# Kernel optimization log

Measured on AMD Instinct MI355X. Metric: run time of the kernel, lower is better.

## Reference

```python
import jax, jax.numpy as jnp
import numpy as np

N_NODES = 50000
N_EDGES = 20000
EDGE_SIZE = 32
IN_CH = 256
OUT_CH = 256


def setup_inputs() -> dict:
    key = jax.random.key(0)
    k1, k2, k3 = jax.random.split(key, 3)
    x = jax.random.normal(k1, (N_NODES, IN_CH), dtype=jnp.float32)
    hyperedges = jax.random.randint(k2, (N_EDGES, EDGE_SIZE), 0, N_NODES)
    weight = jax.random.normal(k3, (IN_CH, OUT_CH), dtype=jnp.float32)
    return {"x": x, "hyperedges": hyperedges, "weight": weight}


def reference(x, hyperedges, weight):
    # Gather node features per hyperedge and reduce ('sum' aggregation):
    # [E, K, C] -> [E, C]
    edge_sum = x[hyperedges].sum(axis=1)
    # Scatter-add each hyperedge's summed feature back to every member node.
    agg = jnp.zeros_like(x).at[hyperedges].add(edge_sum[:, None, :])
    # Dense projection + ReLU.
    return jax.nn.relu(agg @ weight)
```

## Files before the change

kernel.cpp:

```cpp
#include <hip/hip_runtime.h>
#include <hip/hip_bf16.h>

#define N_NODES 50000
#define N_EDGES 20000
#define EDGE_K  32
#define CH      256
#define N_INC   (N_EDGES * EDGE_K)
#define ELL_CAP 64

typedef __attribute__((ext_vector_type(4))) float f32x4;
typedef __attribute__((ext_vector_type(8))) short bf16x8;

static __device__ __forceinline__ unsigned short f2bf(float f) {
    __hip_bfloat16 h = __float2bfloat16(f);
    return *reinterpret_cast<unsigned short*>(&h);
}

static __device__ __forceinline__ float bf2f(unsigned short u) {
    unsigned int b = ((unsigned int)u) << 16;
    float f;
    __builtin_memcpy(&f, &b, 4);
    return f;
}

#define CONV_BLOCKS ((N_NODES * CH / 4 + 255) / 256)
#define ZERO_BLOCKS ((N_NODES + 255) / 256)
__global__ void prep_kernel(const float* __restrict__ x, unsigned short* __restrict__ xb,
                            const float* __restrict__ w, unsigned short* __restrict__ wt,
                            int* __restrict__ deg) {
    int b = blockIdx.x;
    if (b < CONV_BLOCKS) {
        int i = b * 256 + threadIdx.x;
        if (i < N_NODES * CH / 4) {
            f32x4 v = reinterpret_cast<const f32x4*>(x)[i];
            ushort4 s;
            s.x = f2bf(v.x);
            s.y = f2bf(v.y);
            s.z = f2bf(v.z);
            s.w = f2bf(v.w);
            reinterpret_cast<ushort4*>(xb)[i] = s;
        }
    } else if (b < CONV_BLOCKS + CH) {
        int n = b - CONV_BLOCKS;
        int k = threadIdx.x;
        wt[n * CH + k] = f2bf(w[k * CH + n]);
    } else {
        int i = (b - CONV_BLOCKS - CH) * 256 + threadIdx.x;
        if (i < N_NODES) deg[i] = 0;
    }
}

#define GATHER_BLOCKS ((N_EDGES + 3) / 4)
#define FILL_BLOCKS   ((N_INC + 255) / 256)
__global__ void gather_fill_kernel(const unsigned short* __restrict__ xb,
                                   const int* __restrict__ he,
                                   unsigned short* __restrict__ es,
                                   int* __restrict__ deg,
                                   unsigned short* __restrict__ ell) {
    int b = blockIdx.x;
    if (b < GATHER_BLOCKS) {
        int wave = b * 4 + (threadIdx.x >> 6);
        int lane = threadIdx.x & 63;
        if (wave >= N_EDGES) return;
        int myidx = he[wave * EDGE_K + (lane & 31)];
        const ushort4* xb4 = reinterpret_cast<const ushort4*>(xb);
        f32x4 acc = {0.f, 0.f, 0.f, 0.f};
#pragma unroll
        for (int k = 0; k < EDGE_K; ++k) {
            int e = __shfl(myidx, k, 64);
            ushort4 v = xb4[(size_t)e * (CH / 4) + lane];
            acc.x += bf2f(v.x);
            acc.y += bf2f(v.y);
            acc.z += bf2f(v.z);
            acc.w += bf2f(v.w);
        }
        ushort4 s;
        s.x = f2bf(acc.x);
        s.y = f2bf(acc.y);
        s.z = f2bf(acc.z);
        s.w = f2bf(acc.w);
        reinterpret_cast<ushort4*>(es + (size_t)wave * CH)[lane] = s;
    } else {
        int i = (b - GATHER_BLOCKS) * 256 + threadIdx.x;
        if (i >= N_INC) return;
        int node = he[i];
        int slot = atomicAdd(&deg[node], 1);
        if (slot < ELL_CAP) ell[(size_t)node * ELL_CAP + slot] = (unsigned short)(i >> 5);
    }
}

__global__ __launch_bounds__(256) void gemm_kernel(const unsigned short* __restrict__ es,
                                                   const unsigned short* __restrict__ wt,
                                                   unsigned short* __restrict__ yb) {
    int wid  = threadIdx.x >> 6;
    int lane = threadIdx.x & 63;
    int m0   = blockIdx.x * 64 + wid * 16;
    if (m0 >= N_EDGES) return;
    int lr = lane & 15;
    int lg = lane >> 4;

    f32x4 acc[16] = {};

    const unsigned short* arow = es + (size_t)(m0 + lr) * CH + lg * 8;
#pragma unroll
    for (int kk = 0; kk < CH; kk += 32) {
        bf16x8 a = *reinterpret_cast<const bf16x8*>(arow + kk);
#pragma unroll
        for (int nt = 0; nt < 16; ++nt) {
            bf16x8 b = *reinterpret_cast<const bf16x8*>(
                wt + (size_t)(nt * 16 + lr) * CH + kk + lg * 8);
            acc[nt] = __builtin_amdgcn_mfma_f32_16x16x32_bf16(a, b, acc[nt], 0, 0, 0);
        }
    }

#pragma unroll
    for (int nt = 0; nt < 16; ++nt) {
#pragma unroll
        for (int r = 0; r < 4; ++r) {
            yb[(size_t)(m0 + lg * 4 + r) * CH + nt * 16 + lr] = f2bf(acc[nt][r]);
        }
    }
}

__global__ void apply_kernel(const unsigned short* __restrict__ yb, const int* __restrict__ deg,
                             const unsigned short* __restrict__ ell, float* __restrict__ out) {
    int node = (int)((blockIdx.x * blockDim.x + threadIdx.x) >> 6);
    int lane = threadIdx.x & 63;
    if (node >= N_NODES) return;
    int d = deg[node];
    if (d > ELL_CAP) d = ELL_CAP;
    int myidx = (int)ell[(size_t)node * ELL_CAP + lane];
    const ushort4* yb4 = reinterpret_cast<const ushort4*>(yb);
    f32x4 acc = {0.f, 0.f, 0.f, 0.f};
    int j = 0;
    for (; j + 4 <= d; j += 4) {
        int e0 = __shfl(myidx, j + 0, 64);
        int e1 = __shfl(myidx, j + 1, 64);
        int e2 = __shfl(myidx, j + 2, 64);
        int e3 = __shfl(myidx, j + 3, 64);
        ushort4 v0 = yb4[(size_t)e0 * (CH / 4) + lane];
        ushort4 v1 = yb4[(size_t)e1 * (CH / 4) + lane];
        ushort4 v2 = yb4[(size_t)e2 * (CH / 4) + lane];
        ushort4 v3 = yb4[(size_t)e3 * (CH / 4) + lane];
        acc.x += bf2f(v0.x) + bf2f(v1.x) + bf2f(v2.x) + bf2f(v3.x);
        acc.y += bf2f(v0.y) + bf2f(v1.y) + bf2f(v2.y) + bf2f(v3.y);
        acc.z += bf2f(v0.z) + bf2f(v1.z) + bf2f(v2.z) + bf2f(v3.z);
        acc.w += bf2f(v0.w) + bf2f(v1.w) + bf2f(v2.w) + bf2f(v3.w);
    }
    for (; j < d; ++j) {
        int e = __shfl(myidx, j, 64);
        ushort4 v = yb4[(size_t)e * (CH / 4) + lane];
        acc.x += bf2f(v.x);
        acc.y += bf2f(v.y);
        acc.z += bf2f(v.z);
        acc.w += bf2f(v.w);
    }
    acc.x = fmaxf(acc.x, 0.f);
    acc.y = fmaxf(acc.y, 0.f);
    acc.z = fmaxf(acc.z, 0.f);
    acc.w = fmaxf(acc.w, 0.f);
    reinterpret_cast<f32x4*>(out + (size_t)node * CH)[lane] = acc;
}

extern "C" void kernel_launch(void* const* d_in, const int* in_sizes, int n_in,
                              void* d_out, int out_size, void* d_ws, size_t ws_size,
                              hipStream_t stream) {
    const float* x  = (const float*)d_in[0];
    const int*   he = (const int*)d_in[1];
    const float* w  = (const float*)d_in[2];
    float* out = (float*)d_out;

    char* ws = (char*)d_ws;
    unsigned short* wt  = (unsigned short*)ws;
    unsigned short* es  = (unsigned short*)(ws + 131072);
    unsigned short* yb  = (unsigned short*)(ws + 131072 + 10240000);
    int* deg = (int*)(ws + 131072 + 10240000 + 10240000);
    unsigned short* ell = (unsigned short*)(ws + 131072 + 10240000 + 10240000 + 200000);

    unsigned short* xb = (unsigned short*)d_out;

    prep_kernel<<<CONV_BLOCKS + CH + ZERO_BLOCKS, 256, 0, stream>>>(x, xb, w, wt, deg);

    gather_fill_kernel<<<GATHER_BLOCKS + FILL_BLOCKS, 256, 0, stream>>>(xb, he, es, deg, ell);

    {
        int blocks = (N_EDGES + 63) / 64;
        gemm_kernel<<<blocks, 256, 0, stream>>>(es, wt, yb);
    }

    {
        int blocks = (N_NODES + 3) / 4;
        apply_kernel<<<blocks, 256, 0, stream>>>(yb, deg, ell, out);
    }
}
```

Baseline: 164.1 us.

## Fuse node aggregation with GEMM and partition ELL fill by node groups

Removes the separate edge-side GEMM and its intermediate buffer. A new kernel first gathers each node's incident hyperedge sums into shared memory. It then runs the projection with MFMA and applies ReLU before writing the output. The ELL fill is split into windows that each handle one of eight node ranges, so atomics land in a smaller region, at the cost of reading the hyperedge list eight times. The GEMM now runs over 50000 nodes instead of 20000 edges, and the output stores are narrower per lane.

New measurement: 184.3 us. +12.3%, slower.

```diff
diff --git a/kernel.cpp b/kernel.cpp
--- a/kernel.cpp
+++ b/kernel.cpp
@@ -50,16 +50,34 @@
     }
 }
 
+#define FILL_GROUPS   8
+#define NODES_PER_GRP (N_NODES / FILL_GROUPS)
+#define FILL_WIN      2560
+#define FILL_BLOCKS   ((N_INC / FILL_WIN) * FILL_GROUPS)
 #define GATHER_BLOCKS ((N_EDGES + 3) / 4)
-#define FILL_BLOCKS   ((N_INC + 255) / 256)
 __global__ void gather_fill_kernel(const unsigned short* __restrict__ xb,
                                    const int* __restrict__ he,
                                    unsigned short* __restrict__ es,
                                    int* __restrict__ deg,
                                    unsigned short* __restrict__ ell) {
     int b = blockIdx.x;
-    if (b < GATHER_BLOCKS) {
-        int wave = b * 4 + (threadIdx.x >> 6);
+    if (b < FILL_BLOCKS) {
+        int g  = b % FILL_GROUPS;
+        int wn = b / FILL_GROUPS;
+        int lo = g * NODES_PER_GRP, hi = lo + NODES_PER_GRP;
+        int base = wn * FILL_WIN;
+#pragma unroll
+        for (int it = 0; it < FILL_WIN / 256; ++it) {
+            int i = base + it * 256 + threadIdx.x;
+            int node = he[i];
+            if (node >= lo && node < hi) {
+                int slot = atomicAdd(&deg[node], 1);
+                if (slot < ELL_CAP)
+                    ell[(size_t)node * ELL_CAP + slot] = (unsigned short)(i >> 5);
+            }
+        }
+    } else {
+        int wave = (b - FILL_BLOCKS) * 4 + (threadIdx.x >> 6);
         int lane = threadIdx.x & 63;
         if (wave >= N_EDGES) return;
         int myidx = he[wave * EDGE_K + (lane & 31)];
@@ -80,86 +98,91 @@
         s.z = f2bf(acc.z);
         s.w = f2bf(acc.w);
         reinterpret_cast<ushort4*>(es + (size_t)wave * CH)[lane] = s;
-    } else {
-        int i = (b - GATHER_BLOCKS) * 256 + threadIdx.x;
-        if (i >= N_INC) return;
-        int node = he[i];
-        int slot = atomicAdd(&deg[node], 1);
-        if (slot < ELL_CAP) ell[(size_t)node * ELL_CAP + slot] = (unsigned short)(i >> 5);
-    }
-}
-
-__global__ __launch_bounds__(256) void gemm_kernel(const unsigned short* __restrict__ es,
-                                                   const unsigned short* __restrict__ wt,
-                                                   unsigned short* __restrict__ yb) {
-    int wid  = threadIdx.x >> 6;
+    }
+}
+
+#define AP_NODES 32
+#define ZPAD     264
+__global__ __launch_bounds__(256) void apply_gemm_kernel(const unsigned short* __restrict__ es,
+                                                         const unsigned short* __restrict__ wt,
+                                                         const int* __restrict__ deg,
+                                                         const unsigned short* __restrict__ ell,
+                                                         float* __restrict__ out) {
+    __shared__ unsigned short zs[AP_NODES * ZPAD];
+    int w    = threadIdx.x >> 6;
     int lane = threadIdx.x & 63;
-    int m0   = blockIdx.x * 64 + wid * 16;
-    if (m0 >= N_EDGES) return;
+    int nbase = blockIdx.x * AP_NODES;
+
+    const ushort4* es4 = reinterpret_cast<const ushort4*>(es);
+    for (int t = 0; t < 8; ++t) {
+        int local = w * 8 + t;
+        int node  = nbase + local;
+        int nr    = node < N_NODES ? node : N_NODES - 1;
+        int d     = node < N_NODES ? deg[nr] : 0;
+        if (d > ELL_CAP) d = ELL_CAP;
+        int myidx = (int)ell[(size_t)nr * ELL_CAP + lane];
+        f32x4 acc = {0.f, 0.f, 0.f, 0.f};
+        int j = 0;
+        for (; j + 4 <= d; j += 4) {
+            int e0 = __shfl(myidx, j + 0, 64);
+            int e1 = __shfl(myidx, j + 1, 64);
+            int e2 = __shfl(myidx, j + 2, 64);
+            int e3 = __shfl(myidx, j + 3, 64);
+            ushort4 v0 = es4[(size_t)e0 * (CH / 4) + lane];
+            ushort4 v1 = es4[(size_t)e1 * (CH / 4) + lane];
+            ushort4 v2 = es4[(size_t)e2 * (CH / 4) + lane];
+            ushort4 v3 = es4[(size_t)e3 * (CH / 4) + lane];
+            acc.x += bf2f(v0.x) + bf2f(v1.x) + bf2f(v2.x) + bf2f(v3.x);
+            acc.y += bf2f(v0.y) + bf2f(v1.y) + bf2f(v2.y) + bf2f(v3.y);
+            acc.z += bf2f(v0.z) + bf2f(v1.z) + bf2f(v2.z) + bf2f(v3.z);
+            acc.w += bf2f(v0.w) + bf2f(v1.w) + bf2f(v2.w) + bf2f(v3.w);
+        }
+        for (; j < d; ++j) {
+            int e = __shfl(myidx, j, 64);
+            ushort4 v = es4[(size_t)e * (CH / 4) + lane];
+            acc.x += bf2f(v.x);
+            acc.y += bf2f(v.y);
+            acc.z += bf2f(v.z);
+            acc.w += bf2f(v.w);
+        }
+        ushort4 s;
+        s.x = f2bf(acc.x);
+        s.y = f2bf(acc.y);
+        s.z = f2bf(acc.z);
+        s.w = f2bf(acc.w);
+        *reinterpret_cast<ushort4*>(&zs[local * ZPAD + lane * 4]) = s;
+    }
+    __syncthreads();
+
+    int strip = w >> 1;
+    int half  = w & 1;
     int lr = lane & 15;
     int lg = lane >> 4;
 
-    f32x4 acc[16] = {};
-
-    const unsigned short* arow = es + (size_t)(m0 + lr) * CH + lg * 8;
+    f32x4 acc[8] = {};
+    const unsigned short* zrow = &zs[(strip * 16 + lr) * ZPAD + lg * 8];
 #pragma unroll
     for (int kk = 0; kk < CH; kk += 32) {
-        bf16x8 a = *reinterpret_cast<const bf16x8*>(arow + kk);
-#pragma unroll
-        for (int nt = 0; nt < 16; ++nt) {
-            bf16x8 b = *reinterpret_cast<const bf16x8*>(
-                wt + (size_t)(nt * 16 + lr) * CH + kk + lg * 8);
-            acc[nt] = __builtin_amdgcn_mfma_f32_16x16x32_bf16(a, b, acc[nt], 0, 0, 0);
-        }
-    }
-
-#pragma unroll
-    for (int nt = 0; nt < 16; ++nt) {
+        bf16x8 a = *reinterpret_cast<const bf16x8*>(zrow + kk);
+#pragma unroll
+        for (int nt = 0; nt < 8; ++nt) {
+            bf16x8 bb = *reinterpret_cast<const bf16x8*>(
+                wt + (size_t)((half * 8 + nt) * 16 + lr) * CH + kk + lg * 8);
+            acc[nt] = __builtin_amdgcn_mfma_f32_16x16x32_bf16(a, bb, acc[nt], 0, 0, 0);
+        }
+    }
+
+#pragma unroll
+    for (int nt = 0; nt < 8; ++nt) {
 #pragma unroll
         for (int r = 0; r < 4; ++r) {
-            yb[(size_t)(m0 + lg * 4 + r) * CH + nt * 16 + lr] = f2bf(acc[nt][r]);
-        }
-    }
-}
-
-__global__ void apply_kernel(const unsigned short* __restrict__ yb, const int* __restrict__ deg,
-                             const unsigned short* __restrict__ ell, float* __restrict__ out) {
-    int node = (int)((blockIdx.x * blockDim.x + threadIdx.x) >> 6);
-    int lane = threadIdx.x & 63;
-    if (node >= N_NODES) return;
-    int d = deg[node];
-    if (d > ELL_CAP) d = ELL_CAP;
-    int myidx = (int)ell[(size_t)node * ELL_CAP + lane];
-    const ushort4* yb4 = reinterpret_cast<const ushort4*>(yb);
-    f32x4 acc = {0.f, 0.f, 0.f, 0.f};
-    int j = 0;
-    for (; j + 4 <= d; j += 4) {
-        int e0 = __shfl(myidx, j + 0, 64);
-        int e1 = __shfl(myidx, j + 1, 64);
-        int e2 = __shfl(myidx, j + 2, 64);
-        int e3 = __shfl(myidx, j + 3, 64);
-        ushort4 v0 = yb4[(size_t)e0 * (CH / 4) + lane];
-        ushort4 v1 = yb4[(size_t)e1 * (CH / 4) + lane];
-        ushort4 v2 = yb4[(size_t)e2 * (CH / 4) + lane];
-        ushort4 v3 = yb4[(size_t)e3 * (CH / 4) + lane];
-        acc.x += bf2f(v0.x) + bf2f(v1.x) + bf2f(v2.x) + bf2f(v3.x);
-        acc.y += bf2f(v0.y) + bf2f(v1.y) + bf2f(v2.y) + bf2f(v3.y);
-        acc.z += bf2f(v0.z) + bf2f(v1.z) + bf2f(v2.z) + bf2f(v3.z);
-        acc.w += bf2f(v0.w) + bf2f(v1.w) + bf2f(v2.w) + bf2f(v3.w);
-    }
-    for (; j < d; ++j) {
-        int e = __shfl(myidx, j, 64);
-        ushort4 v = yb4[(size_t)e * (CH / 4) + lane];
-        acc.x += bf2f(v.x);
-        acc.y += bf2f(v.y);
-        acc.z += bf2f(v.z);
-        acc.w += bf2f(v.w);
-    }
-    acc.x = fmaxf(acc.x, 0.f);
-    acc.y = fmaxf(acc.y, 0.f);
-    acc.z = fmaxf(acc.z, 0.f);
-    acc.w = fmaxf(acc.w, 0.f);
-    reinterpret_cast<f32x4*>(out + (size_t)node * CH)[lane] = acc;
+            int node = nbase + strip * 16 + lg * 4 + r;
+            if (node < N_NODES) {
+                float v = acc[nt][r];
+                out[(size_t)node * CH + (half * 8 + nt) * 16 + lr] = fmaxf(v, 0.f);
+            }
+        }
+    }
 }
 
 extern "C" void kernel_launch(void* const* d_in, const int* in_sizes, int n_in,
@@ -173,23 +196,17 @@
     char* ws = (char*)d_ws;
     unsigned short* wt  = (unsigned short*)ws;
     unsigned short* es  = (unsigned short*)(ws + 131072);
-    unsigned short* yb  = (unsigned short*)(ws + 131072 + 10240000);
-    int* deg = (int*)(ws + 131072 + 10240000 + 10240000);
-    unsigned short* ell = (unsigned short*)(ws + 131072 + 10240000 + 10240000 + 200000);
+    int* deg = (int*)(ws + 131072 + 10240000);
+    unsigned short* ell = (unsigned short*)(ws + 131072 + 10240000 + 200000);
 
     unsigned short* xb = (unsigned short*)d_out;
 
     prep_kernel<<<CONV_BLOCKS + CH + ZERO_BLOCKS, 256, 0, stream>>>(x, xb, w, wt, deg);
 
-    gather_fill_kernel<<<GATHER_BLOCKS + FILL_BLOCKS, 256, 0, stream>>>(xb, he, es, deg, ell);
+    gather_fill_kernel<<<FILL_BLOCKS + GATHER_BLOCKS, 256, 0, stream>>>(xb, he, es, deg, ell);
 
     {
-        int blocks = (N_EDGES + 63) / 64;
-        gemm_kernel<<<blocks, 256, 0, stream>>>(es, wt, yb);
-    }
-
-    {
-        int blocks = (N_NODES + 3) / 4;
-        apply_kernel<<<blocks, 256, 0, stream>>>(yb, deg, ell, out);
-    }
-}
+        int blocks = (N_NODES + AP_NODES - 1) / AP_NODES;
+        apply_gemm_kernel<<<blocks, 256, 0, stream>>>(es, wt, deg, ell, out);
+    }
+}
```
